# Performance work log

Measured on AMD Instinct MI355X. Metric: run time of the kernel, lower is better.

Reference implementation:

```python
import jax, jax.numpy as jnp
import numpy as np

N_NODES = 50000
N_EDGES = 800000
NODE_IN_DIM = 768
NODE_DIM = 512
OUTPUT_NUM = 97
B, P = 8, 2048


def setup_inputs() -> dict:
    key = jax.random.key(0)
    ks = jax.random.split(key, 10)
    node_features = jax.random.normal(ks[0], (N_NODES, NODE_IN_DIM), jnp.float32)
    edge_features = jax.random.normal(ks[1], (N_EDGES, 32), jnp.float32)
    src = jax.random.randint(ks[2], (N_EDGES,), 0, N_NODES)
    dst = jax.random.randint(ks[3], (N_EDGES,), 0, N_NODES)
    head_ent_nodes = jax.random.randint(ks[4], (B, P), 0, N_NODES)
    tail_ent_nodes = jax.random.randint(ks[5], (B, P), 0, N_NODES)
    # params (xavier-ish scale for weights)
    W1 = jax.random.normal(ks[6], (NODE_IN_DIM, NODE_DIM), jnp.float32) / np.sqrt(NODE_IN_DIM)
    b1 = jax.random.normal(ks[7], (NODE_DIM,), jnp.float32) * 0.01
    Wp = jax.random.normal(ks[8], (2 * NODE_DIM, OUTPUT_NUM), jnp.float32) / np.sqrt(2 * NODE_DIM)
    bp = jax.random.normal(ks[9], (OUTPUT_NUM,), jnp.float32) * 0.01
    return {
        "node_features": node_features, "edge_features": edge_features,
        "W1": W1, "b1": b1, "Wp": Wp, "bp": bp,
        "src": src, "dst": dst,
        "head_ent_nodes": head_ent_nodes, "tail_ent_nodes": tail_ent_nodes,
    }


def reference(node_features, edge_features, W1, b1, Wp, bp, src, dst, head_ent_nodes, tail_ent_nodes):
    n = node_features.shape[0]
    # node_fc: Linear + ReLU
    h = jax.nn.relu(node_features @ W1 + b1)  # [N, D]
    # DGL update_all: message = dst node's own h, mean-reduced at dst.
    # (src is part of the graph but unused by this message function.)
    msg = h[dst]  # [E, D] gather
    agg = jax.ops.segment_sum(msg, dst, num_segments=n)  # [N, D]
    deg = jax.ops.segment_sum(jnp.ones((dst.shape[0],), h.dtype), dst, num_segments=n)  # [N]
    # nodes with no incoming messages keep their old h (DGL UDF semantics)
    h_new = jnp.where((deg > 0)[:, None], agg / jnp.maximum(deg, 1.0)[:, None], h)
    head = h_new[head_ent_nodes]  # [B, P, D]
    tail = h_new[tail_ent_nodes]  # [B, P, D]
    out = jnp.concatenate([head, tail], axis=2) @ Wp + bp  # [B, P, 97]
    return out
```

## Files before the change

### kernel.cpp

```cpp
#include <hip/hip_runtime.h>
#include <hip/hip_bf16.h>
#include <stdint.h>

using bf16x8 = __attribute__((ext_vector_type(8))) short;
using f32x4  = __attribute__((ext_vector_type(4))) float;

#define N_NODES  50000
#define K1       768
#define D1       512
#define NPAIR    16384
#define NOUT     97
#define NOUT_PAD 112
#define MTILES   391
#define NTILES   4
#define NWG      (MTILES * NTILES)
#define WGPX     196
#define KSTEPS   (K1 / 32)

__device__ __forceinline__ uint16_t f2bf(float f) {
    uint32_t u = __builtin_bit_cast(uint32_t, f);
    return (uint16_t)((u + 0x7fffu + ((u >> 16) & 1u)) >> 16);
}

__device__ __forceinline__ uint32_t cvt_pk_bf16(float lo, float hi) {
    uint32_t r;
    asm("v_cvt_pk_bf16_f32 %0, %1, %2" : "=v"(r) : "v"(lo), "v"(hi));
    return r;
}

__device__ __forceinline__ void gll16(const void* g, void* l) {
    __builtin_amdgcn_global_load_lds(
        (const __attribute__((address_space(1))) void*)g,
        (__attribute__((address_space(3))) void*)l, 16, 0, 0);
}

__global__ void k_convert(const float* __restrict__ W1, const float* __restrict__ Wp,
                          uint16_t* __restrict__ W1t, uint16_t* __restrict__ Wpt) {
    int idx = blockIdx.x * 256 + threadIdx.x;
    const int n1 = D1 * K1;
    if (idx < n1) {
        int c = idx / K1, k = idx - c * K1;
        W1t[idx] = f2bf(W1[k * D1 + c]);
    } else {
        int j = idx - n1;
        if (j < NOUT_PAD * 1024) {
            int c = j >> 10, k = j & 1023;
            Wpt[j] = (c < NOUT) ? f2bf(Wp[k * NOUT + c]) : (uint16_t)0;
        }
    }
}

__global__ __launch_bounds__(512) void k_gemm1(const float* __restrict__ A,
        const uint16_t* __restrict__ W1t, const float* __restrict__ bias1,
        uint16_t* __restrict__ H) {
    __shared__ float    lds_a[2 * 4096];
    __shared__ uint16_t lds_b[2 * 4096];

    const int bid = blockIdx.x;
    const int tt = (bid & 7) * WGPX + (bid >> 3);
    if (tt >= NWG) return;
    const int m0 = (tt >> 2) * 128, n0 = (tt & 3) * 128;

    const int t = threadIdx.x, lane = t & 63, w = t >> 6;
    const int wm = w >> 1, wn = w & 1;
    const int cl = lane & 15, kh = lane >> 4;

    const float* aSrc[2];
    #pragma unroll
    for (int i = 0; i < 2; ++i) {
        int r = m0 + i * 64 + (t >> 3);
        if (r >= N_NODES) r = N_NODES - 1;
        aSrc[i] = A + (size_t)r * K1 + (((t & 7) ^ ((t >> 3) & 7)) * 4);
    }
    const uint16_t* bSrc =
        W1t + (size_t)(n0 + (t >> 2)) * K1 + (((t & 3) ^ ((t >> 3) & 3)) * 8);

    float*    aDst = &lds_a[w * 256];
    uint16_t* bDst = &lds_b[w * 512];

    const int q7 = cl & 7;
    const int pa0 = ((2 * kh) ^ q7) * 4, pa1 = ((2 * kh + 1) ^ q7) * 4;
    const int arow0 = (wm * 32 + cl) * 32;
    const int brow0 = (wn * 64 + cl) * 32 + ((kh ^ ((cl >> 1) & 3)) * 8);

    f32x4 acc[2][4];
    const f32x4 z = {0.f, 0.f, 0.f, 0.f};
    #pragma unroll
    for (int m = 0; m < 2; ++m)
        #pragma unroll
        for (int n = 0; n < 4; ++n) acc[m][n] = z;

#define STAGE(BUF) do {                                                        \
    gll16(aSrc[0], aDst + (BUF) * 4096);                                       \
    gll16(aSrc[1], aDst + (BUF) * 4096 + 2048);                                \
    gll16(bSrc,    bDst + (BUF) * 4096);                                       \
    aSrc[0] += 32; aSrc[1] += 32; bSrc += 32;                                  \
    } while (0)

#define COMPUTE(BUF) do {                                                      \
    const float*    la = &lds_a[(BUF) * 4096];                                 \
    const uint16_t* lb = &lds_b[(BUF) * 4096];                                 \
    bf16x8 bfr[4];                                                             \
    _Pragma("unroll")                                                          \
    for (int n = 0; n < 4; ++n)                                                \
        bfr[n] = *(const bf16x8*)&lb[brow0 + n * 512];                         \
    _Pragma("unroll")                                                          \
    for (int m = 0; m < 2; ++m) {                                              \
        f32x4 r0 = *(const f32x4*)&la[arow0 + m * 512 + pa0];                  \
        f32x4 r1 = *(const f32x4*)&la[arow0 + m * 512 + pa1];                  \
        uint32_t uu[4];                                                        \
        uu[0] = cvt_pk_bf16(r0[0], r0[1]);                                     \
        uu[1] = cvt_pk_bf16(r0[2], r0[3]);                                     \
        uu[2] = cvt_pk_bf16(r1[0], r1[1]);                                     \
        uu[3] = cvt_pk_bf16(r1[2], r1[3]);                                     \
        bf16x8 af = *(const bf16x8*)uu;                                        \
        _Pragma("unroll")                                                      \
        for (int n = 0; n < 4; ++n)                                            \
            acc[m][n] = __builtin_amdgcn_mfma_f32_16x16x32_bf16(               \
                            af, bfr[n], acc[m][n], 0, 0, 0);                   \
    }                                                                          \
    } while (0)

    STAGE(0);
    for (int kt = 0; kt < KSTEPS - 1; ++kt) {
        const int cur = kt & 1;
        STAGE(cur ^ 1);
        asm volatile("s_waitcnt vmcnt(3)" ::: "memory");
        __builtin_amdgcn_s_barrier();
        COMPUTE(cur);
        __builtin_amdgcn_s_barrier();
    }
    asm volatile("s_waitcnt vmcnt(0)" ::: "memory");
    __builtin_amdgcn_s_barrier();
    COMPUTE((KSTEPS - 1) & 1);

#undef STAGE
#undef COMPUTE

    float bv[4]; int bcol[4];
    #pragma unroll
    for (int n = 0; n < 4; ++n) { bcol[n] = n0 + wn * 64 + n * 16 + cl; bv[n] = bias1[bcol[n]]; }
    #pragma unroll
    for (int m = 0; m < 2; ++m) {
        int rbase = m0 + wm * 32 + m * 16 + kh * 4;
        #pragma unroll
        for (int rr = 0; rr < 4; ++rr) {
            int row = rbase + rr;
            if (row < N_NODES) {
                #pragma unroll
                for (int n = 0; n < 4; ++n) {
                    float v = acc[m][n][rr] + bv[n];
                    H[(size_t)row * D1 + bcol[n]] = f2bf(fmaxf(v, 0.f));
                }
            }
        }
    }
}

__global__ __launch_bounds__(256) void k_gemm2(const uint16_t* __restrict__ H,
        const uint16_t* __restrict__ Wpt, const float* __restrict__ bp,
        const int* __restrict__ head, const int* __restrict__ tail,
        float* __restrict__ out) {
    __shared__ uint16_t lds_w[NOUT_PAD][40];
    const int t = threadIdx.x;
    const int lane = t & 63, wave = t >> 6;
    const int cl = lane & 15, kh = lane >> 4;
    const int rowbase = blockIdx.x * 64 + wave * 16;
    const int i_l = rowbase + cl;
    const int nodeH = head[i_l], nodeT = tail[i_l];
    const uint16_t* hH = H + (size_t)nodeH * D1 + kh * 8;
    const uint16_t* hT = H + (size_t)nodeT * D1 + kh * 8;

    f32x4 acc[7];
    const f32x4 z = {0.f, 0.f, 0.f, 0.f};
    #pragma unroll
    for (int n = 0; n < 7; ++n) acc[n] = z;

    const int wrow = t >> 1, whalf = t & 1;
    const uint16_t* wsrc = Wpt + (size_t)wrow * 1024 + whalf * 16;
    uint16_t* wdst = &lds_w[wrow][whalf * 16];

    for (int kb = 0; kb < 32; ++kb) {
        uint4 w0 = {0,0,0,0}, w1 = {0,0,0,0};
        if (t < 224) {
            const uint4* wp4 = (const uint4*)(wsrc + kb * 32);
            w0 = wp4[0]; w1 = wp4[1];
        }
        bf16x8 af = (kb < 16) ? *(const bf16x8*)(hH + kb * 32)
                              : *(const bf16x8*)(hT + (kb - 16) * 32);
        __syncthreads();
        if (t < 224) { ((uint4*)wdst)[0] = w0; ((uint4*)wdst)[1] = w1; }
        __syncthreads();
        #pragma unroll
        for (int n = 0; n < 7; ++n) {
            bf16x8 bfr = *(const bf16x8*)&lds_w[n * 16 + cl][kh * 8];
            acc[n] = __builtin_amdgcn_mfma_f32_16x16x32_bf16(af, bfr, acc[n], 0, 0, 0);
        }
    }
    #pragma unroll
    for (int n = 0; n < 7; ++n) {
        int col = n * 16 + cl;
        if (col < NOUT) {
            float bb = bp[col];
            #pragma unroll
            for (int rr = 0; rr < 4; ++rr) {
                int i = rowbase + kh * 4 + rr;
                out[(size_t)i * NOUT + col] = acc[n][rr] + bb;
            }
        }
    }
}

extern "C" void kernel_launch(void* const* d_in, const int* in_sizes, int n_in,
                              void* d_out, int out_size, void* d_ws, size_t ws_size,
                              hipStream_t stream) {
    const float* node_features = (const float*)d_in[0];
    const float* W1   = (const float*)d_in[2];
    const float* b1   = (const float*)d_in[3];
    const float* Wp   = (const float*)d_in[4];
    const float* bp   = (const float*)d_in[5];
    const int* head   = (const int*)d_in[8];
    const int* tail   = (const int*)d_in[9];
    float* out = (float*)d_out;

    char* ws = (char*)d_ws;
    uint16_t* H   = (uint16_t*)ws;
    uint16_t* W1t = (uint16_t*)(ws + (size_t)N_NODES * D1 * 2);
    uint16_t* Wpt = (uint16_t*)(ws + (size_t)N_NODES * D1 * 2 + (size_t)D1 * K1 * 2);

    const int convN = D1 * K1 + NOUT_PAD * 1024;
    k_convert<<<(convN + 255) / 256, 256, 0, stream>>>(W1, Wp, W1t, Wpt);

    k_gemm1<<<WGPX * 8, 512, 0, stream>>>(node_features, W1t, b1, H);

    k_gemm2<<<NPAIR / 64, 256, 0, stream>>>(H, Wpt, bp, head, tail, out);
}
```

Measured before the change: 99.75 us.

## Retile GEMM1 to full-width 64-row blocks with register-staged bf16 A conversion

GEMM1 now uses 64x512 tiles (one workgroup covers all output columns for 64 rows), so the fp32 node features are read from global memory once instead of four times across column tiles. A is loaded into registers, converted to bf16 and written to LDS, with a two-stage prefetch, while W1 tiles are streamed with global_load_lds. The per-step conversion moves out of the MFMA inner loop and LDS traffic for A is halved. In exchange each step loads the whole W1 k-slice, there are more barriers and manual waitcnt bookkeeping, and the grid has fewer, heavier workgroups.

```diff
diff --git a/kernel.cpp b/kernel.cpp
--- a/kernel.cpp
+++ b/kernel.cpp
@@ -11,21 +11,13 @@
 #define NPAIR    16384
 #define NOUT     97
 #define NOUT_PAD 112
-#define MTILES   391
-#define NTILES   4
-#define NWG      (MTILES * NTILES)
-#define WGPX     196
-#define KSTEPS   (K1 / 32)
+#define BM       64
+#define MT       782
+#define KSTEPS   24
 
 __device__ __forceinline__ uint16_t f2bf(float f) {
     uint32_t u = __builtin_bit_cast(uint32_t, f);
     return (uint16_t)((u + 0x7fffu + ((u >> 16) & 1u)) >> 16);
-}
-
-__device__ __forceinline__ uint32_t cvt_pk_bf16(float lo, float hi) {
-    uint32_t r;
-    asm("v_cvt_pk_bf16_f32 %0, %1, %2" : "=v"(r) : "v"(lo), "v"(hi));
-    return r;
 }
 
 __device__ __forceinline__ void gll16(const void* g, void* l) {
@@ -50,99 +42,128 @@
     }
 }
 
-__global__ __launch_bounds__(512) void k_gemm1(const float* __restrict__ A,
+__global__ __launch_bounds__(512, 4) void k_gemm1(const float* __restrict__ A,
         const uint16_t* __restrict__ W1t, const float* __restrict__ bias1,
         uint16_t* __restrict__ H) {
-    __shared__ float    lds_a[2 * 4096];
-    __shared__ uint16_t lds_b[2 * 4096];
+    __shared__ uint16_t lds_a[2][BM * 32];
+    __shared__ uint16_t lds_b[2][D1 * 32];
 
     const int bid = blockIdx.x;
-    const int tt = (bid & 7) * WGPX + (bid >> 3);
-    if (tt >= NWG) return;
-    const int m0 = (tt >> 2) * 128, n0 = (tt & 3) * 128;
-
-    const int t = threadIdx.x, lane = t & 63, w = t >> 6;
-    const int wm = w >> 1, wn = w & 1;
+    const int m0 = bid * BM;
+    const int t = threadIdx.x, lane = t & 63, wv = t >> 6;
     const int cl = lane & 15, kh = lane >> 4;
 
-    const float* aSrc[2];
-    #pragma unroll
-    for (int i = 0; i < 2; ++i) {
-        int r = m0 + i * 64 + (t >> 3);
-        if (r >= N_NODES) r = N_NODES - 1;
-        aSrc[i] = A + (size_t)r * K1 + (((t & 7) ^ ((t >> 3) & 7)) * 4);
-    }
-    const uint16_t* bSrc =
-        W1t + (size_t)(n0 + (t >> 2)) * K1 + (((t & 3) ^ ((t >> 3) & 3)) * 8);
-
-    float*    aDst = &lds_a[w * 256];
-    uint16_t* bDst = &lds_b[w * 512];
-
-    const int q7 = cl & 7;
-    const int pa0 = ((2 * kh) ^ q7) * 4, pa1 = ((2 * kh + 1) ^ q7) * 4;
-    const int arow0 = (wm * 32 + cl) * 32;
-    const int brow0 = (wn * 64 + cl) * 32 + ((kh ^ ((cl >> 1) & 3)) * 8);
-
-    f32x4 acc[2][4];
+    int arow_g = m0 + (t >> 3); if (arow_g >= N_NODES) arow_g = N_NODES - 1;
+    const float4* aSrc = (const float4*)(A + (size_t)arow_g * K1) + (t & 7);
+    uint16_t* aWr = &lds_a[0][(t >> 3) * 32 + ((((t & 7) >> 1) ^ ((t >> 4) & 3)) * 8) + (t & 1) * 4];
+
+    const uint16_t* bBase = W1t + (size_t)(t >> 2) * K1 + (((t & 3) ^ ((t >> 3) & 3)) * 8);
+
+    const int fo = (kh ^ ((cl >> 1) & 3)) * 8;
+
+    f32x4 acc[4][4];
     const f32x4 z = {0.f, 0.f, 0.f, 0.f};
     #pragma unroll
-    for (int m = 0; m < 2; ++m)
+    for (int m = 0; m < 4; ++m)
         #pragma unroll
         for (int n = 0; n < 4; ++n) acc[m][n] = z;
 
-#define STAGE(BUF) do {                                                        \
-    gll16(aSrc[0], aDst + (BUF) * 4096);                                       \
-    gll16(aSrc[1], aDst + (BUF) * 4096 + 2048);                                \
-    gll16(bSrc,    bDst + (BUF) * 4096);                                       \
-    aSrc[0] += 32; aSrc[1] += 32; bSrc += 32;                                  \
+#define STAGE_B(K, BUF) do {                                                   \
+    _Pragma("unroll")                                                          \
+    for (int i_ = 0; i_ < 4; ++i_)                                             \
+        gll16(bBase + (size_t)i_ * (128 * K1) + (K) * 32,                      \
+              &lds_b[BUF][i_ * 4096 + wv * 512]);                              \
+    } while (0)
+
+#define WRITE_A(BUF, R) do {                                                   \
+    uint32_t lo_ = (uint32_t)f2bf((R).x) | ((uint32_t)f2bf((R).y) << 16);      \
+    uint32_t hi_ = (uint32_t)f2bf((R).z) | ((uint32_t)f2bf((R).w) << 16);      \
+    uint2 v_ = {lo_, hi_};                                                     \
+    *(uint2*)(aWr + (BUF) * (BM * 32)) = v_;                                   \
     } while (0)
 
 #define COMPUTE(BUF) do {                                                      \
-    const float*    la = &lds_a[(BUF) * 4096];                                 \
-    const uint16_t* lb = &lds_b[(BUF) * 4096];                                 \
-    bf16x8 bfr[4];                                                             \
-    _Pragma("unroll")                                                          \
-    for (int n = 0; n < 4; ++n)                                                \
-        bfr[n] = *(const bf16x8*)&lb[brow0 + n * 512];                         \
-    _Pragma("unroll")                                                          \
-    for (int m = 0; m < 2; ++m) {                                              \
-        f32x4 r0 = *(const f32x4*)&la[arow0 + m * 512 + pa0];                  \
-        f32x4 r1 = *(const f32x4*)&la[arow0 + m * 512 + pa1];                  \
-        uint32_t uu[4];                                                        \
-        uu[0] = cvt_pk_bf16(r0[0], r0[1]);                                     \
-        uu[1] = cvt_pk_bf16(r0[2], r0[3]);                                     \
-        uu[2] = cvt_pk_bf16(r1[0], r1[1]);                                     \
-        uu[3] = cvt_pk_bf16(r1[2], r1[3]);                                     \
-        bf16x8 af = *(const bf16x8*)uu;                                        \
+    const uint16_t* la_ = &lds_a[BUF][0];                                      \
+    const uint16_t* lb_ = &lds_b[BUF][0];                                      \
+    bf16x8 af_[4], bq_[4];                                                     \
+    _Pragma("unroll")                                                          \
+    for (int mf = 0; mf < 4; ++mf)                                             \
+        af_[mf] = *(const bf16x8*)&la_[(mf * 16 + cl) * 32 + fo];              \
+    _Pragma("unroll")                                                          \
+    for (int nf = 0; nf < 4; ++nf)                                             \
+        bq_[nf] = *(const bf16x8*)&lb_[(wv * 64 + nf * 16 + cl) * 32 + fo];    \
+    _Pragma("unroll")                                                          \
+    for (int mf = 0; mf < 4; ++mf)                                             \
         _Pragma("unroll")                                                      \
-        for (int n = 0; n < 4; ++n)                                            \
-            acc[m][n] = __builtin_amdgcn_mfma_f32_16x16x32_bf16(               \
-                            af, bfr[n], acc[m][n], 0, 0, 0);                   \
-    }                                                                          \
-    } while (0)
-
-    STAGE(0);
-    for (int kt = 0; kt < KSTEPS - 1; ++kt) {
-        const int cur = kt & 1;
-        STAGE(cur ^ 1);
-        asm volatile("s_waitcnt vmcnt(3)" ::: "memory");
+        for (int nf = 0; nf < 4; ++nf)                                         \
+            acc[mf][nf] = __builtin_amdgcn_mfma_f32_16x16x32_bf16(             \
+                              af_[mf], bq_[nf], acc[mf][nf], 0, 0, 0);         \
+    } while (0)
+
+#define READS_DONE_BARRIER() do {                                              \
+    __builtin_amdgcn_sched_barrier(0);                                         \
+    asm volatile("s_waitcnt lgkmcnt(0)" ::: "memory");                         \
+    __builtin_amdgcn_s_barrier();                                              \
+    } while (0)
+
+    float4 rA0 = aSrc[0];
+    float4 rA1 = aSrc[8];
+    STAGE_B(0, 0);
+    STAGE_B(1, 1);
+    WRITE_A(0, rA0);
+    rA0 = aSrc[16];
+    WRITE_A(1, rA1);
+    rA1 = aSrc[24];
+    asm volatile("s_waitcnt vmcnt(6)" ::: "memory");
+    asm volatile("s_waitcnt lgkmcnt(0)" ::: "memory");
+    __builtin_amdgcn_s_barrier();
+
+    for (int ktc = 0; ktc < 20; ++ktc) {
+        COMPUTE(ktc & 1);
+        READS_DONE_BARRIER();
+        STAGE_B(ktc + 2, ktc & 1);
+        WRITE_A(ktc & 1, rA0);
+        rA0 = rA1;
+        rA1 = aSrc[(ktc + 4) * 8];
+        asm volatile("s_waitcnt vmcnt(6)" ::: "memory");
+        asm volatile("s_waitcnt lgkmcnt(0)" ::: "memory");
         __builtin_amdgcn_s_barrier();
-        COMPUTE(cur);
-        __builtin_amdgcn_s_barrier();
-    }
+    }
+    COMPUTE(0);
+    READS_DONE_BARRIER();
+    STAGE_B(22, 0);
+    WRITE_A(0, rA0);
+    rA0 = rA1;
+    asm volatile("s_waitcnt vmcnt(5)" ::: "memory");
+    asm volatile("s_waitcnt lgkmcnt(0)" ::: "memory");
+    __builtin_amdgcn_s_barrier();
+
+    COMPUTE(1);
+    READS_DONE_BARRIER();
+    STAGE_B(23, 1);
+    WRITE_A(1, rA0);
+    asm volatile("s_waitcnt vmcnt(4)" ::: "memory");
+    asm volatile("s_waitcnt lgkmcnt(0)" ::: "memory");
+    __builtin_amdgcn_s_barrier();
+
+    COMPUTE(0);
+    READS_DONE_BARRIER();
     asm volatile("s_waitcnt vmcnt(0)" ::: "memory");
     __builtin_amdgcn_s_barrier();
-    COMPUTE((KSTEPS - 1) & 1);
-
-#undef STAGE
+
+    COMPUTE(1);
+
+#undef STAGE_B
+#undef WRITE_A
 #undef COMPUTE
+#undef READS_DONE_BARRIER
 
     float bv[4]; int bcol[4];
     #pragma unroll
-    for (int n = 0; n < 4; ++n) { bcol[n] = n0 + wn * 64 + n * 16 + cl; bv[n] = bias1[bcol[n]]; }
-    #pragma unroll
-    for (int m = 0; m < 2; ++m) {
-        int rbase = m0 + wm * 32 + m * 16 + kh * 4;
+    for (int n = 0; n < 4; ++n) { bcol[n] = wv * 64 + n * 16 + cl; bv[n] = bias1[bcol[n]]; }
+    #pragma unroll
+    for (int m = 0; m < 4; ++m) {
+        int rbase = m0 + m * 16 + kh * 4;
         #pragma unroll
         for (int rr = 0; rr < 4; ++rr) {
             int row = rbase + rr;
@@ -231,7 +252,7 @@
     const int convN = D1 * K1 + NOUT_PAD * 1024;
     k_convert<<<(convN + 255) / 256, 256, 0, stream>>>(W1, Wp, W1t, Wpt);
 
-    k_gemm1<<<WGPX * 8, 512, 0, stream>>>(node_features, W1t, b1, H);
+    k_gemm1<<<MT, 512, 0, stream>>>(node_features, W1t, b1, H);
 
     k_gemm2<<<NPAIR / 64, 256, 0, stream>>>(H, Wpt, bp, head, tail, out);
 }
```

After: 107.9 us. 8.1% more time.

## Enlarge GEMM1 tile to 128x256 with 4-stage LDS pipeline and MFMA priority

Applied to the files above, without the earlier changes.

The node-projection GEMM now uses 128x256 output tiles, so each wave computes a 64x64 sub-tile and the fp32 A rows are fetched half as often across N. The K loop becomes a 4-deep ring of async global-to-LDS loads with three stages in flight, each compute step followed by a read-done barrier. MFMA issue is wrapped in s_setprio and the A fragments are converted before the MFMA block. The cost is far more LDS per block (about 96 KB), which limits occupancy despite the launch-bounds hint, and there are half as many workgroups.

```diff
diff --git a/kernel.cpp b/kernel.cpp
--- a/kernel.cpp
+++ b/kernel.cpp
@@ -11,11 +11,13 @@
 #define NPAIR    16384
 #define NOUT     97
 #define NOUT_PAD 112
-#define MTILES   391
-#define NTILES   4
-#define NWG      (MTILES * NTILES)
-#define WGPX     196
-#define KSTEPS   (K1 / 32)
+#define BM       128
+#define BN       256
+#define MT1      391
+#define NT2      2
+#define NWG1     (MT1 * NT2)
+#define WGPX1    98
+#define HALVES   24
 
 __device__ __forceinline__ uint16_t f2bf(float f) {
     uint32_t u = __builtin_bit_cast(uint32_t, f);
@@ -50,99 +52,120 @@
     }
 }
 
-__global__ __launch_bounds__(512) void k_gemm1(const float* __restrict__ A,
+__global__ __launch_bounds__(512, 2) void k_gemm1(const float* __restrict__ A,
         const uint16_t* __restrict__ W1t, const float* __restrict__ bias1,
         uint16_t* __restrict__ H) {
-    __shared__ float    lds_a[2 * 4096];
-    __shared__ uint16_t lds_b[2 * 4096];
+    __shared__ float    lds_a[4][BM * 32];
+    __shared__ uint16_t lds_b[4][BN * 32];
 
     const int bid = blockIdx.x;
-    const int tt = (bid & 7) * WGPX + (bid >> 3);
-    if (tt >= NWG) return;
-    const int m0 = (tt >> 2) * 128, n0 = (tt & 3) * 128;
-
-    const int t = threadIdx.x, lane = t & 63, w = t >> 6;
-    const int wm = w >> 1, wn = w & 1;
+    const int tt = (bid & 7) * WGPX1 + (bid >> 3);
+    if (tt >= NWG1) return;
+    const int m0 = (tt >> 1) * BM, n0 = (tt & 1) * BN;
+
+    const int t = threadIdx.x, lane = t & 63, wv = t >> 6;
+    const int wm = wv >> 2, wn = wv & 3;
     const int cl = lane & 15, kh = lane >> 4;
-
-    const float* aSrc[2];
+    const int l3 = lane >> 3, l7 = lane & 7;
+
+    const float* aS[2];
     #pragma unroll
     for (int i = 0; i < 2; ++i) {
-        int r = m0 + i * 64 + (t >> 3);
+        int r = m0 + wv * 16 + i * 8 + l3;
         if (r >= N_NODES) r = N_NODES - 1;
-        aSrc[i] = A + (size_t)r * K1 + (((t & 7) ^ ((t >> 3) & 7)) * 4);
-    }
-    const uint16_t* bSrc =
-        W1t + (size_t)(n0 + (t >> 2)) * K1 + (((t & 3) ^ ((t >> 3) & 3)) * 8);
-
-    float*    aDst = &lds_a[w * 256];
-    uint16_t* bDst = &lds_b[w * 512];
+        aS[i] = A + (size_t)r * K1 + ((l7 ^ l3) * 4);
+    }
+    const uint16_t* bS[2];
+    #pragma unroll
+    for (int i = 0; i < 2; ++i)
+        bS[i] = W1t + (size_t)(n0 + wv * 32 + i * 16 + (lane >> 2)) * K1
+                    + (((lane & 3) ^ ((lane >> 3) & 3)) * 8);
 
     const int q7 = cl & 7;
     const int pa0 = ((2 * kh) ^ q7) * 4, pa1 = ((2 * kh + 1) ^ q7) * 4;
-    const int arow0 = (wm * 32 + cl) * 32;
-    const int brow0 = (wn * 64 + cl) * 32 + ((kh ^ ((cl >> 1) & 3)) * 8);
-
-    f32x4 acc[2][4];
+    const int arow = (wm * 64 + cl) * 32;
+    const int brow = (wn * 64 + cl) * 32 + ((kh ^ ((cl >> 1) & 3)) * 8);
+
+    f32x4 acc[4][4];
     const f32x4 z = {0.f, 0.f, 0.f, 0.f};
     #pragma unroll
-    for (int m = 0; m < 2; ++m)
+    for (int m = 0; m < 4; ++m)
         #pragma unroll
         for (int n = 0; n < 4; ++n) acc[m][n] = z;
 
-#define STAGE(BUF) do {                                                        \
-    gll16(aSrc[0], aDst + (BUF) * 4096);                                       \
-    gll16(aSrc[1], aDst + (BUF) * 4096 + 2048);                                \
-    gll16(bSrc,    bDst + (BUF) * 4096);                                       \
-    aSrc[0] += 32; aSrc[1] += 32; bSrc += 32;                                  \
+#define STAGE(h) do {                                                          \
+    const int b_ = (h) & 3;                                                    \
+    gll16(aS[0] + (h) * 32, &lds_a[b_][wv * 512]);                             \
+    gll16(aS[1] + (h) * 32, &lds_a[b_][wv * 512 + 256]);                       \
+    gll16(bS[0] + (h) * 32, &lds_b[b_][wv * 1024]);                            \
+    gll16(bS[1] + (h) * 32, &lds_b[b_][wv * 1024 + 512]);                      \
     } while (0)
 
-#define COMPUTE(BUF) do {                                                      \
-    const float*    la = &lds_a[(BUF) * 4096];                                 \
-    const uint16_t* lb = &lds_b[(BUF) * 4096];                                 \
-    bf16x8 bfr[4];                                                             \
+#define COMPUTE(h) do {                                                        \
+    const float*    la_ = &lds_a[(h) & 3][0];                                  \
+    const uint16_t* lb_ = &lds_b[(h) & 3][0];                                  \
+    bf16x8 af_[4], bq_[4];                                                     \
     _Pragma("unroll")                                                          \
-    for (int n = 0; n < 4; ++n)                                                \
-        bfr[n] = *(const bf16x8*)&lb[brow0 + n * 512];                         \
+    for (int nf = 0; nf < 4; ++nf)                                             \
+        bq_[nf] = *(const bf16x8*)&lb_[brow + nf * 512];                       \
     _Pragma("unroll")                                                          \
-    for (int m = 0; m < 2; ++m) {                                              \
-        f32x4 r0 = *(const f32x4*)&la[arow0 + m * 512 + pa0];                  \
-        f32x4 r1 = *(const f32x4*)&la[arow0 + m * 512 + pa1];                  \
-        uint32_t uu[4];                                                        \
-        uu[0] = cvt_pk_bf16(r0[0], r0[1]);                                     \
-        uu[1] = cvt_pk_bf16(r0[2], r0[3]);                                     \
-        uu[2] = cvt_pk_bf16(r1[0], r1[1]);                                     \
-        uu[3] = cvt_pk_bf16(r1[2], r1[3]);                                     \
-        bf16x8 af = *(const bf16x8*)uu;                                        \
+    for (int mf = 0; mf < 4; ++mf) {                                           \
+        f32x4 r0 = *(const f32x4*)&la_[arow + mf * 512 + pa0];                 \
+        f32x4 r1 = *(const f32x4*)&la_[arow + mf * 512 + pa1];                 \
+        uint32_t uu_[4];                                                       \
+        uu_[0] = cvt_pk_bf16(r0[0], r0[1]);                                    \
+        uu_[1] = cvt_pk_bf16(r0[2], r0[3]);                                    \
+        uu_[2] = cvt_pk_bf16(r1[0], r1[1]);                                    \
+        uu_[3] = cvt_pk_bf16(r1[2], r1[3]);                                    \
+        af_[mf] = *(const bf16x8*)uu_;                                         \
+    }                                                                          \
+    __builtin_amdgcn_s_setprio(1);                                             \
+    _Pragma("unroll")                                                          \
+    for (int mf = 0; mf < 4; ++mf)                                             \
         _Pragma("unroll")                                                      \
-        for (int n = 0; n < 4; ++n)                                            \
-            acc[m][n] = __builtin_amdgcn_mfma_f32_16x16x32_bf16(               \
-                            af, bfr[n], acc[m][n], 0, 0, 0);                   \
-    }                                                                          \
+        for (int nf = 0; nf < 4; ++nf)                                         \
+            acc[mf][nf] = __builtin_amdgcn_mfma_f32_16x16x32_bf16(             \
+                              af_[mf], bq_[nf], acc[mf][nf], 0, 0, 0);         \
+    __builtin_amdgcn_s_setprio(0);                                             \
     } while (0)
 
-    STAGE(0);
-    for (int kt = 0; kt < KSTEPS - 1; ++kt) {
-        const int cur = kt & 1;
-        STAGE(cur ^ 1);
-        asm volatile("s_waitcnt vmcnt(3)" ::: "memory");
+#define READS_DONE_BARRIER() do {                                              \
+    __builtin_amdgcn_sched_barrier(0);                                         \
+    asm volatile("s_waitcnt lgkmcnt(0)" ::: "memory");                         \
+    __builtin_amdgcn_s_barrier();                                              \
+    } while (0)
+
+    STAGE(0); STAGE(1); STAGE(2);
+
+    for (int h = 0; h < HALVES - 3; ++h) {
+        STAGE(h + 3);
+        asm volatile("s_waitcnt vmcnt(12)" ::: "memory");
         __builtin_amdgcn_s_barrier();
-        COMPUTE(cur);
-        __builtin_amdgcn_s_barrier();
-    }
+        COMPUTE(h);
+        READS_DONE_BARRIER();
+    }
+    asm volatile("s_waitcnt vmcnt(8)" ::: "memory");
+    __builtin_amdgcn_s_barrier();
+    COMPUTE(21);
+    READS_DONE_BARRIER();
+    asm volatile("s_waitcnt vmcnt(4)" ::: "memory");
+    __builtin_amdgcn_s_barrier();
+    COMPUTE(22);
+    READS_DONE_BARRIER();
     asm volatile("s_waitcnt vmcnt(0)" ::: "memory");
     __builtin_amdgcn_s_barrier();
-    COMPUTE((KSTEPS - 1) & 1);
+    COMPUTE(23);
 
 #undef STAGE
 #undef COMPUTE
+#undef READS_DONE_BARRIER
 
     float bv[4]; int bcol[4];
     #pragma unroll
     for (int n = 0; n < 4; ++n) { bcol[n] = n0 + wn * 64 + n * 16 + cl; bv[n] = bias1[bcol[n]]; }
     #pragma unroll
-    for (int m = 0; m < 2; ++m) {
-        int rbase = m0 + wm * 32 + m * 16 + kh * 4;
+    for (int m = 0; m < 4; ++m) {
+        int rbase = m0 + wm * 64 + m * 16 + kh * 4;
         #pragma unroll
         for (int rr = 0; rr < 4; ++rr) {
             int row = rbase + rr;
@@ -231,7 +254,7 @@
     const int convN = D1 * K1 + NOUT_PAD * 1024;
     k_convert<<<(convN + 255) / 256, 256, 0, stream>>>(W1, Wp, W1t, Wpt);
 
-    k_gemm1<<<WGPX * 8, 512, 0, stream>>>(node_features, W1t, b1, H);
+    k_gemm1<<<WGPX1 * 8, 512, 0, stream>>>(node_features, W1t, b1, H);
 
     k_gemm2<<<NPAIR / 64, 256, 0, stream>>>(H, Wpt, bp, head, tail, out);
 }
```

Result: slower. 138.7 us (+39.0%).

## Tile weight transpose via LDS and swap MFMA operands for vectorized epilogue stores

Applied to the files above, without the earlier changes.

The weight convert kernel now transposes 32x32 tiles through shared memory, so global reads and writes are coalesced and stores are packed in pairs. Both GEMMs swap the MFMA A and B operands, which transposes the accumulator layout so each lane holds four consecutive output columns. That lets the epilogues write packed bf16x4 rows of H and float4 rows of the output instead of scattered scalar stores. An extra lgkmcnt wait and a sched_barrier are added before the loop barrier in gemm1, which may cost a little overlap.

```diff
diff --git a/kernel.cpp b/kernel.cpp
--- a/kernel.cpp
+++ b/kernel.cpp
@@ -4,6 +4,7 @@
 
 using bf16x8 = __attribute__((ext_vector_type(8))) short;
 using f32x4  = __attribute__((ext_vector_type(4))) float;
+typedef float f32x4u __attribute__((ext_vector_type(4), aligned(4)));
 
 #define N_NODES  50000
 #define K1       768
@@ -15,7 +16,7 @@
 #define NTILES   4
 #define NWG      (MTILES * NTILES)
 #define WGPX     196
-#define KSTEPS   (K1 / 32)
+#define KSTEPS   24
 
 __device__ __forceinline__ uint16_t f2bf(float f) {
     uint32_t u = __builtin_bit_cast(uint32_t, f);
@@ -34,18 +35,47 @@
         (__attribute__((address_space(3))) void*)l, 16, 0, 0);
 }
 
-__global__ void k_convert(const float* __restrict__ W1, const float* __restrict__ Wp,
-                          uint16_t* __restrict__ W1t, uint16_t* __restrict__ Wpt) {
-    int idx = blockIdx.x * 256 + threadIdx.x;
-    const int n1 = D1 * K1;
-    if (idx < n1) {
-        int c = idx / K1, k = idx - c * K1;
-        W1t[idx] = f2bf(W1[k * D1 + c]);
+__global__ __launch_bounds__(256) void k_convert(const float* __restrict__ W1,
+        const float* __restrict__ Wp, uint16_t* __restrict__ W1t, uint16_t* __restrict__ Wpt) {
+    __shared__ uint16_t lds[32][34];
+    const int t = threadIdx.x;
+    const int b = blockIdx.x;
+    const int lane = t & 31, rw = t >> 5;
+    const int lane16 = t & 15, rw2 = t >> 4;
+
+    if (b < 384) {
+        const int kt = b % 24, ct = b / 24;
+        const int k0 = kt * 32, c0 = ct * 32;
+        #pragma unroll
+        for (int j = 0; j < 4; ++j) {
+            int k = rw + j * 8;
+            lds[lane][k] = f2bf(W1[(size_t)(k0 + k) * D1 + c0 + lane]);
+        }
+        __syncthreads();
+        #pragma unroll
+        for (int j = 0; j < 2; ++j) {
+            int c = rw2 + j * 16;
+            uint32_t v = (uint32_t)lds[c][lane16 * 2] | ((uint32_t)lds[c][lane16 * 2 + 1] << 16);
+            *(uint32_t*)&W1t[(size_t)(c0 + c) * K1 + k0 + lane16 * 2] = v;
+        }
     } else {
-        int j = idx - n1;
-        if (j < NOUT_PAD * 1024) {
-            int c = j >> 10, k = j & 1023;
-            Wpt[j] = (c < NOUT) ? f2bf(Wp[k * NOUT + c]) : (uint16_t)0;
+        const int b2 = b - 384;
+        const int kt = b2 % 32, ct = b2 / 32;
+        const int k0 = kt * 32, c0 = ct * 32;
+        #pragma unroll
+        for (int j = 0; j < 4; ++j) {
+            int k = rw + j * 8;
+            float v = (c0 + lane < NOUT) ? Wp[(size_t)(k0 + k) * NOUT + c0 + lane] : 0.f;
+            lds[lane][k] = f2bf(v);
+        }
+        __syncthreads();
+        #pragma unroll
+        for (int j = 0; j < 2; ++j) {
+            int c = rw2 + j * 16;
+            if (c0 + c < NOUT_PAD) {
+                uint32_t v = (uint32_t)lds[c][lane16 * 2] | ((uint32_t)lds[c][lane16 * 2 + 1] << 16);
+                *(uint32_t*)&Wpt[(size_t)(c0 + c) * 1024 + k0 + lane16 * 2] = v;
+            }
         }
     }
 }
@@ -117,7 +147,7 @@
         _Pragma("unroll")                                                      \
         for (int n = 0; n < 4; ++n)                                            \
             acc[m][n] = __builtin_amdgcn_mfma_f32_16x16x32_bf16(               \
-                            af, bfr[n], acc[m][n], 0, 0, 0);                   \
+                            bfr[n], af, acc[m][n], 0, 0, 0);                   \
     }                                                                          \
     } while (0)
 
@@ -128,6 +158,8 @@
         asm volatile("s_waitcnt vmcnt(3)" ::: "memory");
         __builtin_amdgcn_s_barrier();
         COMPUTE(cur);
+        __builtin_amdgcn_sched_barrier(0);
+        asm volatile("s_waitcnt lgkmcnt(0)" ::: "memory");
         __builtin_amdgcn_s_barrier();
     }
     asm volatile("s_waitcnt vmcnt(0)" ::: "memory");
@@ -137,21 +169,23 @@
 #undef STAGE
 #undef COMPUTE
 
-    float bv[4]; int bcol[4];
-    #pragma unroll
-    for (int n = 0; n < 4; ++n) { bcol[n] = n0 + wn * 64 + n * 16 + cl; bv[n] = bias1[bcol[n]]; }
-    #pragma unroll
-    for (int m = 0; m < 2; ++m) {
-        int rbase = m0 + wm * 32 + m * 16 + kh * 4;
-        #pragma unroll
-        for (int rr = 0; rr < 4; ++rr) {
-            int row = rbase + rr;
-            if (row < N_NODES) {
-                #pragma unroll
-                for (int n = 0; n < 4; ++n) {
-                    float v = acc[m][n][rr] + bv[n];
-                    H[(size_t)row * D1 + bcol[n]] = f2bf(fmaxf(v, 0.f));
-                }
+    float4 bb[4];
+    #pragma unroll
+    for (int nf = 0; nf < 4; ++nf)
+        bb[nf] = *(const float4*)&bias1[n0 + wn * 64 + nf * 16 + kh * 4];
+    #pragma unroll
+    for (int mf = 0; mf < 2; ++mf) {
+        int row = m0 + wm * 32 + mf * 16 + cl;
+        if (row < N_NODES) {
+            uint16_t* hp = H + (size_t)row * D1 + n0 + wn * 64 + kh * 4;
+            #pragma unroll
+            for (int nf = 0; nf < 4; ++nf) {
+                float v0 = fmaxf(acc[mf][nf][0] + bb[nf].x, 0.f);
+                float v1 = fmaxf(acc[mf][nf][1] + bb[nf].y, 0.f);
+                float v2 = fmaxf(acc[mf][nf][2] + bb[nf].z, 0.f);
+                float v3 = fmaxf(acc[mf][nf][3] + bb[nf].w, 0.f);
+                uint2 pk = { cvt_pk_bf16(v0, v1), cvt_pk_bf16(v2, v3) };
+                *(uint2*)(hp + nf * 16) = pk;
             }
         }
     }
@@ -194,19 +228,23 @@
         #pragma unroll
         for (int n = 0; n < 7; ++n) {
             bf16x8 bfr = *(const bf16x8*)&lds_w[n * 16 + cl][kh * 8];
-            acc[n] = __builtin_amdgcn_mfma_f32_16x16x32_bf16(af, bfr, acc[n], 0, 0, 0);
-        }
-    }
+            acc[n] = __builtin_amdgcn_mfma_f32_16x16x32_bf16(bfr, af, acc[n], 0, 0, 0);
+        }
+    }
+
+    float* op = out + (size_t)(rowbase + cl) * NOUT;
     #pragma unroll
     for (int n = 0; n < 7; ++n) {
-        int col = n * 16 + cl;
-        if (col < NOUT) {
-            float bb = bp[col];
+        int cb = n * 16 + kh * 4;
+        if (cb + 3 < NOUT) {
+            float4 bbv = *(const float4*)&bp[cb];
+            f32x4u v = { acc[n][0] + bbv.x, acc[n][1] + bbv.y,
+                         acc[n][2] + bbv.z, acc[n][3] + bbv.w };
+            *(f32x4u*)(op + cb) = v;
+        } else if (cb < NOUT) {
             #pragma unroll
-            for (int rr = 0; rr < 4; ++rr) {
-                int i = rowbase + kh * 4 + rr;
-                out[(size_t)i * NOUT + col] = acc[n][rr] + bb;
-            }
+            for (int rr = 0; rr < 4; ++rr)
+                if (cb + rr < NOUT) op[cb + rr] = acc[n][rr] + bp[cb + rr];
         }
     }
 }
@@ -228,8 +266,7 @@
     uint16_t* W1t = (uint16_t*)(ws + (size_t)N_NODES * D1 * 2);
     uint16_t* Wpt = (uint16_t*)(ws + (size_t)N_NODES * D1 * 2 + (size_t)D1 * K1 * 2);
 
-    const int convN = D1 * K1 + NOUT_PAD * 1024;
-    k_convert<<<(convN + 255) / 256, 256, 0, stream>>>(W1, Wp, W1t, Wpt);
+    k_convert<<<512, 256, 0, stream>>>(W1, Wp, W1t, Wpt);
 
     k_gemm1<<<WGPX * 8, 512, 0, stream>>>(node_features, W1t, b1, H);
 
```

After: 104.7 us. 5.0% more time.
